# Kernel optimization log

Measured on AMD Instinct MI355X. Metric: run time of the kernel, lower is better.

Reference implementation:

```python
import jax, jax.numpy as jnp
import numpy as np

NUM_LAYERS = 2


def setup_inputs() -> dict:
    key = jax.random.key(0)
    k1, k2, k3, k4 = jax.random.split(key, 4)
    N, E, D = 50000, 800000, 100
    features = jax.random.normal(k1, (N, D), dtype=jnp.float32)
    # stacked nn.Linear weights, one [D,D] per layer (no bias)
    W = jax.random.normal(k2, (NUM_LAYERS, D, D), dtype=jnp.float32) * 0.02
    src = jax.random.randint(k3, (E,), 0, N)
    dst = jax.random.randint(k4, (E,), 0, N)
    return {"features": features, "W": W, "src": src, "dst": dst}


def reference(features, W, src, dst):
    N, D = features.shape
    num_layers = W.shape[0]
    inv_lp1 = 1.0 / (num_layers + 1)

    # --- graph preprocessing (mirrors ItemConv.graph setter) ---
    # add self loops (fill_diag 1.0), then row-normalize by inverse degree
    loop = jnp.arange(N)
    src_all = jnp.concatenate([src, loop])  # message sources
    dst_all = jnp.concatenate([dst, loop])  # message destinations (rows of adj_t)
    deg = jax.ops.segment_sum(
        jnp.ones(src_all.shape, dtype=features.dtype), dst_all, num_segments=N
    )
    deg_inv = jnp.where(deg > 0, 1.0 / deg, 0.0)
    w = deg_inv[dst_all]  # per-edge weight: row-normalized, [E+N]

    # --- forward (LightGCN-style conv with linear projections) ---
    avg = features * inv_lp1
    x = features
    for i in range(num_layers):
        x = x @ W[i].T  # nn.Linear(D, D, bias=False)
        # SpMM: out[d] = sum_{e: dst=d} w_e * x[src_e]
        x = jax.ops.segment_sum(w[:, None] * x[src_all], dst_all, num_segments=N)
        # F.normalize(x): L2 along dim=-1 with eps=1e-12 (max-clamped norm)
        norm = jnp.linalg.norm(x, axis=-1, keepdims=True)
        avg = avg + (x / jnp.maximum(norm, 1e-12)) * inv_lp1
    return avg
```

## Files before the change

### kernel.cpp

```cpp
#include <hip/hip_runtime.h>

#define D 100
#define YSTRIDE 128
#define BSHIFT 7
#define BSIZE 128
#define BMASK 127
#define NBKMAX 512
#define EPB 2048
#define DCAP 4096

typedef __attribute__((ext_vector_type(8))) short bf8v;
typedef __attribute__((ext_vector_type(4))) float f4v;

__device__ inline unsigned short f2bf(float f) {
    unsigned u = __float_as_uint(f);
    return (unsigned short)((u + 0x7fffu + ((u >> 16) & 1u)) >> 16);
}
__device__ inline float bflo(unsigned v) { return __uint_as_float(v << 16); }
__device__ inline float bfhi(unsigned v) { return __uint_as_float(v & 0xffff0000u); }
__device__ inline unsigned short pk8(float a, float b) {
    return (unsigned short)(__builtin_amdgcn_cvt_pk_fp8_f32(a, b, 0, false) & 0xffff);
}
__device__ inline float up8lo(unsigned v) { return __builtin_amdgcn_cvt_f32_fp8((int)v, 0); }
__device__ inline float up8hi(unsigned v) { return __builtin_amdgcn_cvt_f32_fp8((int)v, 1); }

__device__ inline void scan512_excl(int* a, int* t, int tid) {
    int v0 = a[2 * tid], v1 = a[2 * tid + 1];
    t[tid] = v0 + v1;
    __syncthreads();
    for (int off = 1; off < 256; off <<= 1) {
        int u = (tid >= off) ? t[tid - off] : 0;
        __syncthreads();
        t[tid] += u;
        __syncthreads();
    }
    int base = (tid ? t[tid - 1] : 0);
    a[2 * tid]     = base;
    a[2 * tid + 1] = base + v0;
    __syncthreads();
}

__global__ __launch_bounds__(256) void k_pre(const float* __restrict__ x0, const float* __restrict__ W,
                                             unsigned* __restrict__ s8, float* __restrict__ Wc,
                                             int* __restrict__ bcnt, const int* __restrict__ dst,
                                             int N, int E, int nbk, int packb, int ablk) {
    __shared__ int lhist[NBKMAX];
    int tid = threadIdx.x;
    int bx = blockIdx.x;

    if (bx < packb) {
        int t = bx * 256 + tid;
        if (t >= N * 32) return;
        int d = t >> 5, q = t & 31;
        unsigned p = 0u;
        if (q < D / 4) {
            float4 v = *(const float4*)(x0 + (long)d * D + q * 4);
            p = (unsigned)pk8(v.x, v.y) | ((unsigned)pk8(v.z, v.w) << 16);
        }
        s8[t] = p;
    } else if (bx < packb + ablk) {
        int base = (bx - packb) * EPB;
        int count = min(EPB, E - base);
        for (int i = tid; i < NBKMAX; i += 256) lhist[i] = 0;
        __syncthreads();
        for (int i = tid; i < count; i += 256) atomicAdd(&lhist[dst[base + i] >> BSHIFT], 1);
        __syncthreads();
        for (int b = tid; b < nbk; b += 256)
            if (lhist[b]) atomicAdd(&bcnt[b], lhist[b]);
    } else {
        int t = (bx - packb - ablk) * 256 + tid;
        if (t >= D * D) return;
        int i = t / D, j = t - i * D;
        const float* w2 = W + D * D + (long)i * D;
        float s = 0.f;
        for (int k = 0; k < D; k++) s += w2[k] * W[(long)k * D + j];
        Wc[t] = s;
    }
}

__global__ __launch_bounds__(256) void k_scanB_prep(const int* __restrict__ bucket_cnt,
                                                    int* __restrict__ bucket_off,
                                                    int* __restrict__ bucket_cur, int nbk, int E,
                                                    const float* __restrict__ W1,
                                                    const float* __restrict__ Wc,
                                                    unsigned short* __restrict__ P, int wtot) {
    int tid = threadIdx.x;
    if (blockIdx.x == 0) {
        __shared__ int a[NBKMAX], t[256];
        a[tid]       = (tid < nbk) ? bucket_cnt[tid] : 0;
        a[tid + 256] = (tid + 256 < nbk) ? bucket_cnt[tid + 256] : 0;
        __syncthreads();
        scan512_excl(a, t, tid);
        if (tid < nbk)       { bucket_off[tid] = a[tid];             bucket_cur[tid] = a[tid]; }
        if (tid + 256 < nbk) { bucket_off[tid + 256] = a[tid + 256]; bucket_cur[tid + 256] = a[tid + 256]; }
        if (tid == 0) bucket_off[nbk] = E;
    } else {
        int t = (blockIdx.x - 1) * 256 + tid;
        if (t >= wtot) return;
        int lane = t & 63;
        int r = t >> 6;
        int kt = r & 3;
        int r2 = r >> 2;
        int nt = r2 % 7;
        int l  = r2 / 7;
        const float* M = (l == 0) ? W1 : Wc;
        int ng = nt * 16 + (lane & 15);
        int k0 = kt * 32 + (lane >> 4) * 8;
        unsigned short u[8];
#pragma unroll
        for (int j = 0; j < 8; j++) {
            int k = k0 + j;
            u[j] = (ng < D && k < D) ? f2bf(M[(long)ng * D + k]) : (unsigned short)0;
        }
        uint4 o;
        o.x = (unsigned)u[0] | ((unsigned)u[1] << 16);
        o.y = (unsigned)u[2] | ((unsigned)u[3] << 16);
        o.z = (unsigned)u[4] | ((unsigned)u[5] << 16);
        o.w = (unsigned)u[6] | ((unsigned)u[7] << 16);
        *(uint4*)(P + (long)t * 8) = o;
    }
}

__global__ __launch_bounds__(256) void k_bucketC(const int* __restrict__ src,
                                                 const int* __restrict__ dst,
                                                 int* __restrict__ bucket_cur,
                                                 unsigned* __restrict__ ebuf, int E, int nbk) {
    __shared__ int lhist[NBKMAX], lstart[NBKMAX], runS[NBKMAX], t[256];
    __shared__ unsigned stage[EPB];
    int tid = threadIdx.x;
    int base = blockIdx.x * EPB;
    int count = min(EPB, E - base);

    for (int i = tid; i < NBKMAX; i += 256) lhist[i] = 0;
    __syncthreads();
    for (int i = tid; i < count; i += 256) atomicAdd(&lhist[dst[base + i] >> BSHIFT], 1);
    __syncthreads();
    for (int i = tid; i < NBKMAX; i += 256) lstart[i] = lhist[i];
    __syncthreads();
    scan512_excl(lstart, t, tid);
    for (int b = tid; b < nbk; b += 256) {
        int c = lhist[b];
        runS[b] = c ? atomicAdd(&bucket_cur[b], c) : 0;
    }
    __syncthreads();
    for (int i = tid; i < NBKMAX; i += 256) lhist[i] = 0;
    __syncthreads();
    for (int i = tid; i < count; i += 256) {
        int dv = dst[base + i];
        int sv = src[base + i];
        int b = dv >> BSHIFT;
        int r = atomicAdd(&lhist[b], 1);
        stage[lstart[b] + r] = ((unsigned)(dv & BMASK) << 16) | (unsigned)sv;
    }
    __syncthreads();
    int wave = tid >> 6, lane = tid & 63;
    for (int b = wave; b < nbk; b += 4) {
        int c = lhist[b], ls = lstart[b], rs = runS[b];
        for (int j = lane; j < c; j += 64) ebuf[rs + j] = stage[ls + j];
    }
}

__global__ __launch_bounds__(256) void k_bucketD(const unsigned* __restrict__ ebuf,
                                                 const int* __restrict__ bucket_off,
                                                 int* __restrict__ col, int* __restrict__ rowptr,
                                                 int N, int nbk, int E) {
    __shared__ int lh[BSIZE], ls[BSIZE];
    __shared__ int colStage[DCAP];
    int b = blockIdx.x;
    int tid = threadIdx.x;
    int beg = bucket_off[b], end = bucket_off[b + 1];
    int cnt = end - beg;

    if (tid < BSIZE) lh[tid] = 0;
    __syncthreads();
    for (int i = tid; i < cnt; i += 256) atomicAdd(&lh[ebuf[beg + i] >> 16], 1);
    __syncthreads();
    if (tid < BSIZE) ls[tid] = lh[tid];
    __syncthreads();
    for (int off = 1; off < BSIZE; off <<= 1) {
        int v = (tid >= off && tid < BSIZE) ? ls[tid - off] : 0;
        __syncthreads();
        if (tid < BSIZE) ls[tid] += v;
        __syncthreads();
    }
    if (tid < BSIZE) ls[tid] -= lh[tid];
    __syncthreads();
    int d0 = b * BSIZE;
    if (tid < BSIZE && d0 + tid < N) rowptr[d0 + tid] = beg + ls[tid];
    if (b == nbk - 1 && tid == 0) rowptr[N] = E;
    if (tid < BSIZE) lh[tid] = 0;
    __syncthreads();
    if (cnt <= DCAP) {
        for (int i = tid; i < cnt; i += 256) {
            unsigned p = ebuf[beg + i];
            int r = p >> 16, s = (int)(p & 0xffffu);
            int k = atomicAdd(&lh[r], 1);
            colStage[ls[r] + k] = s;
        }
        __syncthreads();
        for (int i = tid; i < cnt; i += 256) col[beg + i] = colStage[i];
    } else {
        for (int i = tid; i < cnt; i += 256) {
            unsigned p = ebuf[beg + i];
            int r = p >> 16, s = (int)(p & 0xffffu);
            int k = atomicAdd(&lh[r], 1);
            col[beg + ls[r] + k] = s;
        }
    }
}

__global__ __launch_bounds__(256) void k_spmm(const unsigned short* __restrict__ g8,
                                              const int* __restrict__ rowptr,
                                              const int* __restrict__ col,
                                              const unsigned* __restrict__ self16,
                                              unsigned short* __restrict__ o8,
                                              unsigned* __restrict__ o16,
                                              int write8, int N) {
    int wave = threadIdx.x >> 6;
    int lane = threadIdx.x & 63;
    int d0 = (blockIdx.x * 4 + wave) * 2;
    if (d0 >= N) return;
    int d1 = d0 + 1;
    bool has1 = d1 < N;

    int b0 = __builtin_amdgcn_readfirstlane(rowptr[d0]);
    int e0 = __builtin_amdgcn_readfirstlane(rowptr[d0 + 1]);
    int e1 = has1 ? __builtin_amdgcn_readfirstlane(rowptr[d1 + 1]) : e0;

    float ax0, ay0, ax1, ay1;
    if (self16) {
        unsigned sv0 = self16[(long)d0 * 64 + lane];
        ax0 = bflo(sv0); ay0 = bfhi(sv0);
        unsigned sv1 = self16[(long)(has1 ? d1 : d0) * 64 + lane];
        ax1 = bflo(sv1); ay1 = bfhi(sv1);
    } else {
        unsigned sv0 = g8[(long)d0 * 64 + lane];
        ax0 = up8lo(sv0); ay0 = up8hi(sv0);
        unsigned sv1 = g8[(long)(has1 ? d1 : d0) * 64 + lane];
        ax1 = up8lo(sv1); ay1 = up8hi(sv1);
    }

    for (int win = b0; win < e1; win += 64) {
        int m = e1 - win;
        if (m > 64) m = 64;
        int c = col[win + lane];
        int j = 0;
        for (; j + 8 <= m; j += 8) {
            int s0 = __builtin_amdgcn_readlane(c, j);
            int s1 = __builtin_amdgcn_readlane(c, j + 1);
            int s2 = __builtin_amdgcn_readlane(c, j + 2);
            int s3 = __builtin_amdgcn_readlane(c, j + 3);
            int s4 = __builtin_amdgcn_readlane(c, j + 4);
            int s5 = __builtin_amdgcn_readlane(c, j + 5);
            int s6 = __builtin_amdgcn_readlane(c, j + 6);
            int s7 = __builtin_amdgcn_readlane(c, j + 7);
            unsigned v0 = g8[(long)s0 * 64 + lane];
            unsigned v1 = g8[(long)s1 * 64 + lane];
            unsigned v2 = g8[(long)s2 * 64 + lane];
            unsigned v3 = g8[(long)s3 * 64 + lane];
            unsigned v4 = g8[(long)s4 * 64 + lane];
            unsigned v5 = g8[(long)s5 * 64 + lane];
            unsigned v6 = g8[(long)s6 * 64 + lane];
            unsigned v7 = g8[(long)s7 * 64 + lane];
#pragma unroll
            for (int k = 0; k < 8; k++) {
                unsigned vv = (k == 0) ? v0 : (k == 1) ? v1 : (k == 2) ? v2 : (k == 3) ? v3
                            : (k == 4) ? v4 : (k == 5) ? v5 : (k == 6) ? v6 : v7;
                float w0 = (win + j + k < e0) ? 1.f : 0.f;
                float w1 = 1.f - w0;
                float lx = up8lo(vv), ly = up8hi(vv);
                ax0 += lx * w0; ay0 += ly * w0;
                ax1 += lx * w1; ay1 += ly * w1;
            }
        }
        for (; j < m; j++) {
            int s = __builtin_amdgcn_readlane(c, j);
            unsigned vv = g8[(long)s * 64 + lane];
            float w0 = (win + j < e0) ? 1.f : 0.f;
            float w1 = 1.f - w0;
            float lx = up8lo(vv), ly = up8hi(vv);
            ax0 += lx * w0; ay0 += ly * w0;
            ax1 += lx * w1; ay1 += ly * w1;
        }
    }

    float dinv0 = 1.f / (float)(e0 - b0 + 1);
    float dinv1 = 1.f / (float)(e1 - e0 + 1);
    float rx0 = ax0 * dinv0, ry0 = ay0 * dinv0;
    float rx1 = ax1 * dinv1, ry1 = ay1 * dinv1;

    bool act = lane < (D / 2);
    unsigned p0 = act ? ((unsigned)f2bf(rx0) | ((unsigned)f2bf(ry0) << 16)) : 0u;
    o16[(long)d0 * 64 + lane] = p0;
    if (write8) o8[(long)d0 * 64 + lane] = act ? pk8(rx0, ry0) : (unsigned short)0;
    if (has1) {
        unsigned p1 = act ? ((unsigned)f2bf(rx1) | ((unsigned)f2bf(ry1) << 16)) : 0u;
        o16[(long)d1 * 64 + lane] = p1;
        if (write8) o8[(long)d1 * 64 + lane] = act ? pk8(rx1, ry1) : (unsigned short)0;
    }
}

__global__ __launch_bounds__(256) void k_epi(const unsigned short* __restrict__ u16,
                                             const unsigned short* __restrict__ v16,
                                             const unsigned short* __restrict__ P,
                                             const float* __restrict__ x0,
                                             float invlp1, float* __restrict__ out, int N) {
    int wave = threadIdx.x >> 6;
    int lane = threadIdx.x & 63;
    int quad = lane >> 4;
    int l16  = lane & 15;
    int rowbase = (blockIdx.x * 4 + wave) * 16;
    if (rowbase >= N) return;
    int arow = rowbase + l16;
    if (arow >= N) arow = N - 1;

    bf8v aU[4], aV[4];
    const unsigned short* ur = u16 + (long)arow * YSTRIDE;
    const unsigned short* vr = v16 + (long)arow * YSTRIDE;
#pragma unroll
    for (int kt = 0; kt < 4; kt++) {
        int k0 = kt * 32 + quad * 8;
        union { bf8v v; uint4 u; } a, b;
        a.u = *(const uint4*)(ur + k0);
        b.u = *(const uint4*)(vr + k0);
        aU[kt] = a.v;
        aV[kt] = b.v;
    }

    f4v accU[7], accV[7];
#pragma unroll
    for (int nt = 0; nt < 7; nt++) { accU[nt] = (f4v){0,0,0,0}; accV[nt] = (f4v){0,0,0,0}; }

    const uint4* bp = (const uint4*)P;
#pragma unroll
    for (int nt = 0; nt < 7; nt++) {
#pragma unroll
        for (int kt = 0; kt < 4; kt++) {
            union { uint4 u; bf8v v; } b1, b2;
            b1.u = bp[(nt * 4 + kt) * 64 + lane];
            b2.u = bp[(28 + nt * 4 + kt) * 64 + lane];
            accU[nt] = __builtin_amdgcn_mfma_f32_16x16x32_bf16(aU[kt], b1.v, accU[nt], 0, 0, 0);
            accV[nt] = __builtin_amdgcn_mfma_f32_16x16x32_bf16(aV[kt], b2.v, accV[nt], 0, 0, 0);
        }
    }

    float sU[4], sV[4];
#pragma unroll
    for (int i = 0; i < 4; i++) {
        float nu = 0.f, nv = 0.f;
#pragma unroll
        for (int nt = 0; nt < 7; nt++) {
            nu += accU[nt][i] * accU[nt][i];
            nv += accV[nt][i] * accV[nt][i];
        }
#pragma unroll
        for (int m = 1; m < 16; m <<= 1) {
            nu += __shfl_xor(nu, m);
            nv += __shfl_xor(nv, m);
        }
        sU[i] = invlp1 / fmaxf(sqrtf(nu), 1e-12f);
        sV[i] = invlp1 / fmaxf(sqrtf(nv), 1e-12f);
    }

#pragma unroll
    for (int nt = 0; nt < 7; nt++) {
        int cc = nt * 16 + l16;
        if (cc < D) {
#pragma unroll
            for (int i = 0; i < 4; i++) {
                int rr = rowbase + quad * 4 + i;
                if (rr < N) {
                    long idx = (long)rr * D + cc;
                    out[idx] = x0[idx] * invlp1 + accU[nt][i] * sU[i] + accV[nt][i] * sV[i];
                }
            }
        }
    }
}


extern "C" void kernel_launch(void* const* d_in, const int* in_sizes, int n_in,
                              void* d_out, int out_size, void* d_ws, size_t ws_size,
                              hipStream_t stream) {
    const float* features = (const float*)d_in[0];
    const float* W        = (const float*)d_in[1];
    const int*   src      = (const int*)d_in[2];
    const int*   dstv     = (const int*)d_in[3];

    int N = in_sizes[0] / D;
    int E = in_sizes[2];
    int L = in_sizes[1] / (D * D);
    float invlp1 = 1.f / (float)(L + 1);
    int NBK = (N + BSIZE - 1) >> BSHIFT;

    char*  ws  = (char*)d_ws;
    size_t off = 0;
    auto alloc = [&](size_t bytes) -> void* {
        void* p = (void*)(ws + off);
        off += (bytes + 255) & ~(size_t)255;
        return p;
    };
    unsigned*       s8     = (unsigned*)alloc((size_t)N * 32 * sizeof(unsigned));
    unsigned*       u8     = (unsigned*)alloc((size_t)N * 32 * sizeof(unsigned));
    unsigned*       u16    = (unsigned*)alloc((size_t)N * 64 * sizeof(unsigned));
    unsigned*       v16    = (unsigned*)alloc((size_t)N * 64 * sizeof(unsigned));
    float*          Wc     = (float*)alloc((size_t)D * D * sizeof(float));
    unsigned short* wpack  = (unsigned short*)alloc((size_t)2 * 7 * 4 * 64 * 8 * sizeof(unsigned short));
    unsigned*       ebuf   = (unsigned*)alloc((size_t)E * sizeof(unsigned));
    int*            colb   = (int*)alloc((size_t)E * sizeof(int));
    int*            rowptr = (int*)alloc((size_t)(N + 1) * sizeof(int));
    int*            bcnt   = (int*)alloc((size_t)NBKMAX * sizeof(int));
    int*            boff   = (int*)alloc((size_t)(NBKMAX + 1) * sizeof(int));
    int*            bcur   = (int*)alloc((size_t)NBKMAX * sizeof(int));

    int nebk  = (E + EPB - 1) / EPB;
    int wtot  = 2 * 7 * 4 * 64;
    int packb = (N * 32 + 255) / 256;
    int wcb   = (D * D + 255) / 256;
    int prepb = (wtot + 255) / 256;

    hipMemsetAsync(bcnt, 0, (size_t)NBK * sizeof(int), stream);
    k_pre<<<packb + nebk + wcb, 256, 0, stream>>>(features, W, s8, Wc, bcnt, dstv,
                                                  N, E, NBK, packb, nebk);
    k_scanB_prep<<<1 + prepb, 256, 0, stream>>>(bcnt, boff, bcur, NBK, E, W, Wc, wpack, wtot);
    k_bucketC<<<nebk, 256, 0, stream>>>(src, dstv, bcur, ebuf, E, NBK);
    k_bucketD<<<NBK, 256, 0, stream>>>(ebuf, boff, colb, rowptr, N, NBK, E);

    int spmmblocks = (N + 7) / 8;
    k_spmm<<<spmmblocks, 256, 0, stream>>>((const unsigned short*)s8, rowptr, colb,
                                           (const unsigned*)nullptr,
                                           (unsigned short*)u8, u16, 1, N);
    k_spmm<<<spmmblocks, 256, 0, stream>>>((const unsigned short*)u8, rowptr, colb,
                                           u16, (unsigned short*)nullptr, v16, 0, N);

    int nrowtiles = (N + 15) / 16;
    int epiblocks = (nrowtiles + 3) / 4;
    k_epi<<<epiblocks, 256, 0, stream>>>((const unsigned short*)u16, (const unsigned short*)v16,
                                         wpack, features, invlp1, (float*)d_out, N);
}
```

Before: 211.8 us.

## Split SpMM wave into four edge groups with 8-byte gathers per lane

```diff
diff --git a/kernel.cpp b/kernel.cpp
--- a/kernel.cpp
+++ b/kernel.cpp
@@ -23,6 +23,17 @@
 }
 __device__ inline float up8lo(unsigned v) { return __builtin_amdgcn_cvt_f32_fp8((int)v, 0); }
 __device__ inline float up8hi(unsigned v) { return __builtin_amdgcn_cvt_f32_fp8((int)v, 1); }
+
+__device__ inline void acc8(float* acc, uint2 v, float w) {
+    acc[0] = fmaf(__builtin_amdgcn_cvt_f32_fp8((int)v.x, 0), w, acc[0]);
+    acc[1] = fmaf(__builtin_amdgcn_cvt_f32_fp8((int)v.x, 1), w, acc[1]);
+    acc[2] = fmaf(__builtin_amdgcn_cvt_f32_fp8((int)v.x, 2), w, acc[2]);
+    acc[3] = fmaf(__builtin_amdgcn_cvt_f32_fp8((int)v.x, 3), w, acc[3]);
+    acc[4] = fmaf(__builtin_amdgcn_cvt_f32_fp8((int)v.y, 0), w, acc[4]);
+    acc[5] = fmaf(__builtin_amdgcn_cvt_f32_fp8((int)v.y, 1), w, acc[5]);
+    acc[6] = fmaf(__builtin_amdgcn_cvt_f32_fp8((int)v.y, 2), w, acc[6]);
+    acc[7] = fmaf(__builtin_amdgcn_cvt_f32_fp8((int)v.y, 3), w, acc[7]);
+}
 
 __device__ inline void scan512_excl(int* a, int* t, int tid) {
     int v0 = a[2 * tid], v1 = a[2 * tid + 1];
@@ -218,85 +229,80 @@
                                               int write8, int N) {
     int wave = threadIdx.x >> 6;
     int lane = threadIdx.x & 63;
-    int d0 = (blockIdx.x * 4 + wave) * 2;
-    if (d0 >= N) return;
-    int d1 = d0 + 1;
-    bool has1 = d1 < N;
-
-    int b0 = __builtin_amdgcn_readfirstlane(rowptr[d0]);
-    int e0 = __builtin_amdgcn_readfirstlane(rowptr[d0 + 1]);
-    int e1 = has1 ? __builtin_amdgcn_readfirstlane(rowptr[d1 + 1]) : e0;
-
-    float ax0, ay0, ax1, ay1;
-    if (self16) {
-        unsigned sv0 = self16[(long)d0 * 64 + lane];
-        ax0 = bflo(sv0); ay0 = bfhi(sv0);
-        unsigned sv1 = self16[(long)(has1 ? d1 : d0) * 64 + lane];
-        ax1 = bflo(sv1); ay1 = bfhi(sv1);
+    int g = lane >> 4;
+    int j = lane & 15;
+    int d = blockIdx.x * 4 + wave;
+    if (d >= N) return;
+
+    int b0 = __builtin_amdgcn_readfirstlane(rowptr[d]);
+    int e0 = __builtin_amdgcn_readfirstlane(rowptr[d + 1]);
+
+    float acc[8];
+    if (g == 0) {
+        if (self16) {
+            uint4 sv = *((const uint4*)(self16 + (long)d * 64) + j);
+            acc[0] = bflo(sv.x); acc[1] = bfhi(sv.x);
+            acc[2] = bflo(sv.y); acc[3] = bfhi(sv.y);
+            acc[4] = bflo(sv.z); acc[5] = bfhi(sv.z);
+            acc[6] = bflo(sv.w); acc[7] = bfhi(sv.w);
+        } else {
+            uint2 sv = *(const uint2*)(g8 + (long)d * 64 + j * 4);
+#pragma unroll
+            for (int k = 0; k < 8; k++) acc[k] = 0.f;
+            acc8(acc, sv, 1.f);
+        }
     } else {
-        unsigned sv0 = g8[(long)d0 * 64 + lane];
-        ax0 = up8lo(sv0); ay0 = up8hi(sv0);
-        unsigned sv1 = g8[(long)(has1 ? d1 : d0) * 64 + lane];
-        ax1 = up8lo(sv1); ay1 = up8hi(sv1);
-    }
-
-    for (int win = b0; win < e1; win += 64) {
-        int m = e1 - win;
+#pragma unroll
+        for (int k = 0; k < 8; k++) acc[k] = 0.f;
+    }
+
+    for (int win = b0; win < e0; win += 64) {
+        int m = e0 - win;
         if (m > 64) m = 64;
         int c = col[win + lane];
-        int j = 0;
-        for (; j + 8 <= m; j += 8) {
-            int s0 = __builtin_amdgcn_readlane(c, j);
-            int s1 = __builtin_amdgcn_readlane(c, j + 1);
-            int s2 = __builtin_amdgcn_readlane(c, j + 2);
-            int s3 = __builtin_amdgcn_readlane(c, j + 3);
-            int s4 = __builtin_amdgcn_readlane(c, j + 4);
-            int s5 = __builtin_amdgcn_readlane(c, j + 5);
-            int s6 = __builtin_amdgcn_readlane(c, j + 6);
-            int s7 = __builtin_amdgcn_readlane(c, j + 7);
-            unsigned v0 = g8[(long)s0 * 64 + lane];
-            unsigned v1 = g8[(long)s1 * 64 + lane];
-            unsigned v2 = g8[(long)s2 * 64 + lane];
-            unsigned v3 = g8[(long)s3 * 64 + lane];
-            unsigned v4 = g8[(long)s4 * 64 + lane];
-            unsigned v5 = g8[(long)s5 * 64 + lane];
-            unsigned v6 = g8[(long)s6 * 64 + lane];
-            unsigned v7 = g8[(long)s7 * 64 + lane];
-#pragma unroll
-            for (int k = 0; k < 8; k++) {
-                unsigned vv = (k == 0) ? v0 : (k == 1) ? v1 : (k == 2) ? v2 : (k == 3) ? v3
-                            : (k == 4) ? v4 : (k == 5) ? v5 : (k == 6) ? v6 : v7;
-                float w0 = (win + j + k < e0) ? 1.f : 0.f;
-                float w1 = 1.f - w0;
-                float lx = up8lo(vv), ly = up8hi(vv);
-                ax0 += lx * w0; ay0 += ly * w0;
-                ax1 += lx * w1; ay1 += ly * w1;
-            }
-        }
-        for (; j < m; j++) {
-            int s = __builtin_amdgcn_readlane(c, j);
-            unsigned vv = g8[(long)s * 64 + lane];
-            float w0 = (win + j < e0) ? 1.f : 0.f;
-            float w1 = 1.f - w0;
-            float lx = up8lo(vv), ly = up8hi(vv);
-            ax0 += lx * w0; ay0 += ly * w0;
-            ax1 += lx * w1; ay1 += ly * w1;
-        }
-    }
-
-    float dinv0 = 1.f / (float)(e0 - b0 + 1);
-    float dinv1 = 1.f / (float)(e1 - e0 + 1);
-    float rx0 = ax0 * dinv0, ry0 = ay0 * dinv0;
-    float rx1 = ax1 * dinv1, ry1 = ay1 * dinv1;
-
-    bool act = lane < (D / 2);
-    unsigned p0 = act ? ((unsigned)f2bf(rx0) | ((unsigned)f2bf(ry0) << 16)) : 0u;
-    o16[(long)d0 * 64 + lane] = p0;
-    if (write8) o8[(long)d0 * 64 + lane] = act ? pk8(rx0, ry0) : (unsigned short)0;
-    if (has1) {
-        unsigned p1 = act ? ((unsigned)f2bf(rx1) | ((unsigned)f2bf(ry1) << 16)) : 0u;
-        o16[(long)d1 * 64 + lane] = p1;
-        if (write8) o8[(long)d1 * 64 + lane] = act ? pk8(rx1, ry1) : (unsigned short)0;
+        int t = 0;
+        for (; t + 8 <= m; t += 8) {
+            int sa = __shfl(c, t + g);
+            int sb = __shfl(c, t + 4 + g);
+            uint2 va = *(const uint2*)(g8 + (long)sa * 64 + j * 4);
+            uint2 vb = *(const uint2*)(g8 + (long)sb * 64 + j * 4);
+            acc8(acc, va, 1.f);
+            acc8(acc, vb, 1.f);
+        }
+        for (; t < m; t += 4) {
+            int rem = m - t;
+            int idx = t + ((g < rem) ? g : 0);
+            int sa = __shfl(c, idx);
+            float w = (g < rem) ? 1.f : 0.f;
+            uint2 va = *(const uint2*)(g8 + (long)sa * 64 + j * 4);
+            acc8(acc, va, w);
+        }
+    }
+
+#pragma unroll
+    for (int k = 0; k < 8; k++) {
+        acc[k] += __shfl_xor(acc[k], 16);
+        acc[k] += __shfl_xor(acc[k], 32);
+    }
+
+    float dinv = 1.f / (float)(e0 - b0 + 1);
+    float r[8];
+#pragma unroll
+    for (int k = 0; k < 8; k++) r[k] = acc[k] * dinv;
+
+    if (g == 0) {
+        uint4 o;
+        o.x = (unsigned)f2bf(r[0]) | ((unsigned)f2bf(r[1]) << 16);
+        o.y = (unsigned)f2bf(r[2]) | ((unsigned)f2bf(r[3]) << 16);
+        o.z = (unsigned)f2bf(r[4]) | ((unsigned)f2bf(r[5]) << 16);
+        o.w = (unsigned)f2bf(r[6]) | ((unsigned)f2bf(r[7]) << 16);
+        *((uint4*)(o16 + (long)d * 64) + j) = o;
+    }
+    if (write8 && g == 1) {
+        uint2 p;
+        p.x = (unsigned)pk8(r[0], r[1]) | ((unsigned)pk8(r[2], r[3]) << 16);
+        p.y = (unsigned)pk8(r[4], r[5]) | ((unsigned)pk8(r[6], r[7]) << 16);
+        *((uint2*)((unsigned*)o8 + (long)d * 32) + j) = p;
     }
 }
 
@@ -426,7 +432,7 @@
     k_bucketC<<<nebk, 256, 0, stream>>>(src, dstv, bcur, ebuf, E, NBK);
     k_bucketD<<<NBK, 256, 0, stream>>>(ebuf, boff, colb, rowptr, N, NBK, E);
 
-    int spmmblocks = (N + 7) / 8;
+    int spmmblocks = (N + 3) / 4;
     k_spmm<<<spmmblocks, 256, 0, stream>>>((const unsigned short*)s8, rowptr, colb,
                                            (const unsigned*)nullptr,
                                            (unsigned short*)u8, u16, 1, N);
```

New measurement: 211.3 us. Within noise of the previous version (-0.3%).
